# Kernel optimization log

Hardware: AMD Instinct MI355X
Metric: run time of the kernel (lower is better)

The kernel has to match this reference:

```python
import jax, jax.numpy as jnp
import numpy as np

CLASS_EMBED_DIM = 128
TOPK = 64
EPS = float(np.finfo(float).eps)
ALPHA = 0.99


def setup_inputs() -> dict:
    key = jax.random.key(0)
    k1, k2, k3 = jax.random.split(key, 3)
    b, n, d = 16, 256, 640  # d = embed_dim + class_embed_dim
    embed_dim, inner_dim = 512, 512
    x = jax.random.normal(k1, (b, n, d), dtype=jnp.float32)
    # kaiming-normal style init: std = sqrt(2 / fan_in)
    std = (2.0 / embed_dim) ** 0.5
    Wq = jax.random.normal(k2, (embed_dim, inner_dim), dtype=jnp.float32) * std
    Wk = jax.random.normal(k3, (embed_dim, inner_dim), dtype=jnp.float32) * std
    alpha = jnp.float32(ALPHA)
    return {"x": x, "Wq": Wq, "Wk": Wk, "alpha": alpha}


def reference(x, Wq, Wk, alpha):
    b, n, d = x.shape
    xf = x.reshape(b * n, d)            # (N, embed+class)
    xe = xf[:, :-CLASS_EMBED_DIM]       # (N, embed)
    q = xe @ Wq                         # (N, inner)
    k = xe @ Wk                         # (N, inner)
    D = q.shape[1]
    # dots[i,j] = mean_d (q_i - k_j)^2, via expansion (avoids N x N x D tensor)
    q2 = jnp.sum(q * q, axis=1)
    k2 = jnp.sum(k * k, axis=1)
    dots = (q2[:, None] + k2[None, :] - 2.0 * (q @ k.T)) / D  # (N, N)
    N = dots.shape[0]
    _, idx = jax.lax.top_k(dots, TOPK)  # largest, matching torch.topk
    mask = jnp.zeros_like(dots).at[jnp.arange(N)[:, None], idx].set(1.0)
    mask = ((mask + mask.T) > 0).astype(jnp.float32)
    attn = dots * mask
    A = jnp.eye(N, dtype=dots.dtype) - alpha * attn + EPS
    out = jnp.linalg.inv(A) @ xf        # (N, d); to_v is identity
    return out.reshape(b, n, d)
```

## Files before the change

### kernel.cpp

```cpp
#include <hip/hip_runtime.h>
#include <float.h>

#define NN 4096
#define DD 640
#define DE 512
#define NB 16
#define OB 128
#define NOB (NN/OB)
#define SB 128
#define NSB (NN/SB)

static __device__ __forceinline__ float4 ldg4(const float* p) { return *(const float4*)p; }

__global__ __launch_bounds__(256) void proj_gemm(
    const float* __restrict__ xf, const float* __restrict__ Wq,
    const float* __restrict__ Wk, float* __restrict__ q, float* __restrict__ kk_)
{
  __shared__ float Xs[32][68], Qs[32][68], Ks[32][68];
  const int i0 = blockIdx.x * 64, c0 = blockIdx.y * 64;
  const int t = threadIdx.x, tr = t >> 4, tc = t & 15;
  float accq[4][4] = {}, acck[4][4] = {};
  for (int kb = 0; kb < DE; kb += 32) {
    {
      int m = t >> 3, k4 = (t & 7) << 2;
      float4 v0 = ldg4(xf + (size_t)(i0 + m) * DD + kb + k4);
      float4 v1 = ldg4(xf + (size_t)(i0 + m + 32) * DD + kb + k4);
      Xs[k4+0][m] = v0.x; Xs[k4+1][m] = v0.y; Xs[k4+2][m] = v0.z; Xs[k4+3][m] = v0.w;
      Xs[k4+0][m+32] = v1.x; Xs[k4+1][m+32] = v1.y; Xs[k4+2][m+32] = v1.z; Xs[k4+3][m+32] = v1.w;
    }
    {
      int kr = t >> 3, n8 = (t & 7) << 3;
      *(float4*)&Qs[kr][n8]   = ldg4(Wq + (size_t)(kb + kr) * DE + c0 + n8);
      *(float4*)&Qs[kr][n8+4] = ldg4(Wq + (size_t)(kb + kr) * DE + c0 + n8 + 4);
      *(float4*)&Ks[kr][n8]   = ldg4(Wk + (size_t)(kb + kr) * DE + c0 + n8);
      *(float4*)&Ks[kr][n8+4] = ldg4(Wk + (size_t)(kb + kr) * DE + c0 + n8 + 4);
    }
    __syncthreads();
    #pragma unroll
    for (int kkk = 0; kkk < 32; ++kkk) {
      float a[4], bq[4], bk[4];
      *(float4*)a  = *(const float4*)&Xs[kkk][tr << 2];
      *(float4*)bq = *(const float4*)&Qs[kkk][tc << 2];
      *(float4*)bk = *(const float4*)&Ks[kkk][tc << 2];
      #pragma unroll
      for (int r = 0; r < 4; ++r)
        #pragma unroll
        for (int c = 0; c < 4; ++c) { accq[r][c] += a[r]*bq[c]; acck[r][c] += a[r]*bk[c]; }
    }
    __syncthreads();
  }
  #pragma unroll
  for (int r = 0; r < 4; ++r) {
    float* qp = q   + (size_t)(i0 + (tr<<2) + r) * DE + c0 + (tc<<2);
    float* kp = kk_ + (size_t)(i0 + (tr<<2) + r) * DE + c0 + (tc<<2);
    *(float4*)qp = make_float4(accq[r][0], accq[r][1], accq[r][2], accq[r][3]);
    *(float4*)kp = make_float4(acck[r][0], acck[r][1], acck[r][2], acck[r][3]);
  }
}

__global__ __launch_bounds__(256) void rownorm(
    const float* __restrict__ q, const float* __restrict__ kk_,
    float* __restrict__ q2, float* __restrict__ k2)
{
  int w = (blockIdx.x * 256 + threadIdx.x) >> 6;
  int lane = threadIdx.x & 63;
  const float* src = (w < NN) ? q : kk_;
  int row = (w < NN) ? w : w - NN;
  const float* p = src + (size_t)row * DE;
  float s = 0.f;
  for (int c = lane; c < DE; c += 64) { float v = p[c]; s += v * v; }
  for (int off = 32; off; off >>= 1) s += __shfl_down(s, off);
  if (lane == 0) { if (w < NN) q2[row] = s; else k2[row] = s; }
}

__global__ __launch_bounds__(256) void dots_gemm(
    const float* __restrict__ q, const float* __restrict__ kk_,
    const float* __restrict__ q2, const float* __restrict__ k2,
    float* __restrict__ dots)
{
  __shared__ float Qs[32][68], Ks[32][68];
  const int i0 = blockIdx.x * 64, j0 = blockIdx.y * 64;
  const int t = threadIdx.x, tr = t >> 4, tc = t & 15;
  float acc[4][4] = {};
  for (int kb = 0; kb < DE; kb += 32) {
    int m = t >> 3, k4 = (t & 7) << 2;
    {
      float4 v0 = ldg4(q + (size_t)(i0 + m) * DE + kb + k4);
      float4 v1 = ldg4(q + (size_t)(i0 + m + 32) * DE + kb + k4);
      Qs[k4+0][m] = v0.x; Qs[k4+1][m] = v0.y; Qs[k4+2][m] = v0.z; Qs[k4+3][m] = v0.w;
      Qs[k4+0][m+32] = v1.x; Qs[k4+1][m+32] = v1.y; Qs[k4+2][m+32] = v1.z; Qs[k4+3][m+32] = v1.w;
    }
    {
      float4 v0 = ldg4(kk_ + (size_t)(j0 + m) * DE + kb + k4);
      float4 v1 = ldg4(kk_ + (size_t)(j0 + m + 32) * DE + kb + k4);
      Ks[k4+0][m] = v0.x; Ks[k4+1][m] = v0.y; Ks[k4+2][m] = v0.z; Ks[k4+3][m] = v0.w;
      Ks[k4+0][m+32] = v1.x; Ks[k4+1][m+32] = v1.y; Ks[k4+2][m+32] = v1.z; Ks[k4+3][m+32] = v1.w;
    }
    __syncthreads();
    #pragma unroll
    for (int kkk = 0; kkk < 32; ++kkk) {
      float a[4], b[4];
      *(float4*)a = *(const float4*)&Qs[kkk][tr << 2];
      *(float4*)b = *(const float4*)&Ks[kkk][tc << 2];
      #pragma unroll
      for (int r = 0; r < 4; ++r)
        #pragma unroll
        for (int c = 0; c < 4; ++c) acc[r][c] += a[r]*b[c];
    }
    __syncthreads();
  }
  const float inv = 1.0f / (float)DE;
  float k2v[4]; *(float4*)k2v = ldg4(k2 + j0 + (tc<<2));
  #pragma unroll
  for (int r = 0; r < 4; ++r) {
    float q2v = q2[i0 + (tr<<2) + r];
    float o[4];
    #pragma unroll
    for (int c = 0; c < 4; ++c) o[c] = (q2v + k2v[c] - 2.0f*acc[r][c]) * inv;
    *(float4*)(dots + (size_t)(i0 + (tr<<2) + r) * NN + j0 + (tc<<2)) =
        make_float4(o[0], o[1], o[2], o[3]);
  }
}

__global__ __launch_bounds__(256) void topk_bits(
    const float* __restrict__ dots, unsigned int* __restrict__ bits)
{
  __shared__ float row[NN];
  __shared__ unsigned int b[128];
  __shared__ float rv[4]; __shared__ int ri[4];
  const int i = blockIdx.x, t = threadIdx.x;
  const float* dr = dots + (size_t)i * NN;
  for (int c = t; c < NN; c += 256) row[c] = dr[c];
  if (t < 128) b[t] = 0u;
  __syncthreads();
  for (int it = 0; it < 64; ++it) {
    float bv = -FLT_MAX; int bi = NN;
    for (int c = t; c < NN; c += 256) { float v = row[c]; if (v > bv) { bv = v; bi = c; } }
    for (int off = 32; off; off >>= 1) {
      float ov = __shfl_down(bv, off); int oi = __shfl_down(bi, off);
      if (ov > bv || (ov == bv && oi < bi)) { bv = ov; bi = oi; }
    }
    if ((t & 63) == 0) { rv[t >> 6] = bv; ri[t >> 6] = bi; }
    __syncthreads();
    if (t == 0) {
      float fv = rv[0]; int fi = ri[0];
      for (int w = 1; w < 4; ++w)
        if (rv[w] > fv || (rv[w] == fv && ri[w] < fi)) { fv = rv[w]; fi = ri[w]; }
      b[fi >> 5] |= 1u << (fi & 31);
      row[fi] = -FLT_MAX;
    }
    __syncthreads();
  }
  if (t < 128) bits[(size_t)i * 128 + t] = b[t];
}

__global__ __launch_bounds__(256) void build_A(
    float* __restrict__ A, const unsigned int* __restrict__ bits,
    const float* __restrict__ alpha_p)
{
  int tid = blockIdx.x * 256 + threadIdx.x;
  int i = tid >> 10;
  int j4 = (tid & 1023) << 2;
  float alpha = alpha_p[0];
  float* p = A + (size_t)i * NN + j4;
  float4 d = *(float4*)p;
  unsigned int wrow = bits[(size_t)i * 128 + (j4 >> 5)];
  float dv[4] = {d.x, d.y, d.z, d.w}, o[4];
  #pragma unroll
  for (int u = 0; u < 4; ++u) {
    int j = j4 + u;
    unsigned int m1 = (wrow >> (j & 31)) & 1u;
    unsigned int m2 = (bits[(size_t)j * 128 + (i >> 5)] >> (i & 31)) & 1u;
    float base = (i == j) ? 1.0f : 0.0f;
    o[u] = base - ((m1 | m2) ? alpha * dv[u] : 0.0f);
  }
  *(float4*)p = make_float4(o[0], o[1], o[2], o[3]);
}

__global__ __launch_bounds__(1024) void lu_panel(
    float* __restrict__ A, int k0, int ok0, int* __restrict__ piv)
{
  const int t = threadIdx.x;
  const int M = NN - k0;
  float a[4][NB];
  __shared__ float bufA[NB], bufB[NB];
  __shared__ float rv[16]; __shared__ int ri[16];
  __shared__ int s_pr;
  __shared__ int piv_s[NB];
  __shared__ int sd[32], ss[32];
  __shared__ float l16[16][17];
  __shared__ float gbuf[32][112];

  #pragma unroll
  for (int i = 0; i < 4; ++i) {
    int r = t + (i << 10);
    if (r < M) {
      const float* src = A + (size_t)(k0 + r) * NN + k0;
      #pragma unroll
      for (int c4 = 0; c4 < NB; c4 += 4) {
        float4 v = ldg4(src + c4);
        a[i][c4] = v.x; a[i][c4+1] = v.y; a[i][c4+2] = v.z; a[i][c4+3] = v.w;
      }
    }
  }

  #pragma unroll
  for (int j = 0; j < NB; ++j) {
    float bv = -1.0f; int br = 1 << 30;
    #pragma unroll
    for (int i = 0; i < 4; ++i) {
      int r = t + (i << 10);
      if (r >= j && r < M) {
        float v = fabsf(a[i][j]);
        if (v > bv || (v == bv && r < br)) { bv = v; br = r; }
      }
    }
    for (int off = 32; off; off >>= 1) {
      float ov = __shfl_down(bv, off); int orr = __shfl_down(br, off);
      if (ov > bv || (ov == bv && orr < br)) { bv = ov; br = orr; }
    }
    if ((t & 63) == 0) { rv[t >> 6] = bv; ri[t >> 6] = br; }
    __syncthreads();
    if (t == 0) {
      float fv = rv[0]; int fr = ri[0];
      for (int w = 1; w < 16; ++w)
        if (rv[w] > fv || (rv[w] == fv && ri[w] < fr)) { fv = rv[w]; fr = ri[w]; }
      s_pr = fr; piv_s[j] = k0 + fr;
    }
    __syncthreads();
    const int pr = s_pr, prT = pr & 1023, prS = pr >> 10;
    if (t == prT) {
      #pragma unroll
      for (int i2 = 0; i2 < 4; ++i2) if (i2 == prS) {
        #pragma unroll
        for (int c = 0; c < NB; ++c) bufB[c] = a[i2][c];
      }
    }
    if (t == j) {
      #pragma unroll
      for (int c = 0; c < NB; ++c) bufA[c] = a[0][c];
    }
    __syncthreads();
    if (t == j) {
      #pragma unroll
      for (int c = 0; c < NB; ++c) a[0][c] = bufB[c];
    }
    if (t == prT) {
      #pragma unroll
      for (int i2 = 0; i2 < 4; ++i2) if (i2 == prS) {
        #pragma unroll
        for (int c = 0; c < NB; ++c) a[i2][c] = bufA[c];
      }
    }
    float rp = 1.0f / bufB[j];
    #pragma unroll
    for (int i = 0; i < 4; ++i) {
      int r = t + (i << 10);
      if (r > j && r < M) {
        float mlt = a[i][j] * rp;
        a[i][j] = mlt;
        #pragma unroll
        for (int c = j + 1; c < NB; ++c) a[i][c] -= mlt * bufB[c];
      }
    }
    __syncthreads();
  }

  #pragma unroll
  for (int i = 0; i < 4; ++i) {
    int r = t + (i << 10);
    if (r < M) {
      float* dst = A + (size_t)(k0 + r) * NN + k0;
      #pragma unroll
      for (int c4 = 0; c4 < NB; c4 += 4)
        *(float4*)(dst + c4) = make_float4(a[i][c4], a[i][c4+1], a[i][c4+2], a[i][c4+3]);
    }
  }
  if (t < NB) piv[k0 + t] = piv_s[t];

  if (t < 16) {
    #pragma unroll
    for (int c2 = 0; c2 < NB; ++c2) l16[t][c2] = a[0][c2];
  }

  if (t < 32) {
    int slotrow = (t < NB) ? (k0 + t) : -1;
    int content = slotrow;
    int next_ext = NB;
    for (int j = 0; j < NB; ++j) {
      int p = piv_s[j];
      unsigned long long mask = __ballot(slotrow == p);
      int bslot;
      if (mask) bslot = __ffsll((unsigned long long)mask) - 1;
      else {
        bslot = next_ext;
        if (t == next_ext) { slotrow = p; content = p; }
        next_ext++;
      }
      int srcl = (t == j) ? bslot : ((t == bslot) ? j : t);
      content = __shfl(content, srcl);
    }
    sd[t] = slotrow;
    ss[t] = content;
  }
  __syncthreads();

  const int p16 = k0 - ok0;
  for (int idx = t; idx < 32 * 112; idx += 1024) {
    int i = idx / 112, cc = idx - i * 112;
    if (sd[i] >= 0 && sd[i] != ss[i]) {
      int c = ok0 + (cc < p16 ? cc : cc + NB);
      gbuf[i][cc] = A[(size_t)ss[i] * NN + c];
    }
  }
  __syncthreads();
  for (int idx = t; idx < 32 * 112; idx += 1024) {
    int i = idx / 112, cc = idx - i * 112;
    if (sd[i] >= 0 && sd[i] != ss[i]) {
      int c = ok0 + (cc < p16 ? cc : cc + NB);
      A[(size_t)sd[i] * NN + c] = gbuf[i][cc];
    }
  }
  __syncthreads();

  const int w = ok0 + OB - (k0 + NB);
  if (t < w) {
    int c = k0 + NB + t;
    int cc = p16 + t;
    float x[16];
    #pragma unroll
    for (int i = 0; i < 16; ++i)
      x[i] = (ss[i] != sd[i]) ? gbuf[i][cc] : A[(size_t)(k0 + i) * NN + c];
    #pragma unroll
    for (int i = 1; i < 16; ++i)
      #pragma unroll
      for (int j = 0; j < i; ++j) x[i] -= l16[i][j] * x[j];
    #pragma unroll
    for (int i = 0; i < 16; ++i) A[(size_t)(k0 + i) * NN + c] = x[i];
  }
}

__global__ __launch_bounds__(64) void net_perm128(
    const int* __restrict__ piv_g, int ok0,
    int* __restrict__ nd, int* __restrict__ ns)
{
  __shared__ int pl[OB];
  const int L = threadIdx.x;
  pl[L] = piv_g[ok0 + L];
  pl[L + 64] = piv_g[ok0 + 64 + L];
  __syncthreads();
  int c0 = ok0 + L, c1 = ok0 + 64 + L, c2 = -1, c3 = -1;
  int sr2 = -1, sr3 = -1;
  int next_ext = 128;
  for (int j = 0; j < OB; ++j) {
    int p = pl[j];
    int s2;
    if (p < ok0 + OB) s2 = p - ok0;
    else {
      unsigned long long m2 = __ballot(sr2 == p);
      unsigned long long m3 = __ballot(sr3 == p);
      if (m2) s2 = 128 + (__ffsll(m2) - 1);
      else if (m3) s2 = 192 + (__ffsll(m3) - 1);
      else {
        s2 = next_ext;
        if (s2 < 192) { if (L == s2 - 128) { sr2 = p; c2 = p; } }
        else          { if (L == s2 - 192) { sr3 = p; c3 = p; } }
        next_ext++;
      }
    }
    int jp = j >> 6, jl = j & 63, sp = s2 >> 6, sl = s2 & 63;
    int vj0 = __shfl(c0, jl), vj1 = __shfl(c1, jl);
    int vj = (jp == 0) ? vj0 : vj1;
    int vs0 = __shfl(c0, sl), vs1 = __shfl(c1, sl), vs2 = __shfl(c2, sl), vs3 = __shfl(c3, sl);
    int vs = (sp == 0) ? vs0 : (sp == 1) ? vs1 : (sp == 2) ? vs2 : vs3;
    if (jp == 0 && L == jl) c0 = vs;
    if (jp == 1 && L == jl) c1 = vs;
    if (sp == 0 && L == sl) c0 = vj;
    if (sp == 1 && L == sl) c1 = vj;
    if (sp == 2 && L == sl) c2 = vj;
    if (sp == 3 && L == sl) c3 = vj;
  }
  nd[L] = ok0 + L;        ns[L] = c0;
  nd[64 + L] = ok0 + 64 + L; ns[64 + L] = c1;
  nd[128 + L] = sr2;      ns[128 + L] = c2;
  nd[192 + L] = sr3;      ns[192 + L] = c3;
}

__global__ __launch_bounds__(256) void perm_copy_out(
    const float* __restrict__ A, float* __restrict__ T,
    const int* __restrict__ nd, const int* __restrict__ ns, int ok0)
{
  int s = blockIdx.y;
  int d = nd[s], sr = ns[s];
  if (d < 0 || d == sr) return;
  int c = blockIdx.x * 1024 + threadIdx.x * 4;
  if (c >= ok0 && c < ok0 + OB) return;
  *(float4*)(T + (size_t)s * NN + c) = ldg4(A + (size_t)sr * NN + c);
}

__global__ __launch_bounds__(256) void perm_copy_in(
    float* __restrict__ A, const float* __restrict__ T,
    const int* __restrict__ nd, const int* __restrict__ ns, int ok0)
{
  int s = blockIdx.y;
  int d = nd[s], sr = ns[s];
  if (d < 0 || d == sr) return;
  int c = blockIdx.x * 1024 + threadIdx.x * 4;
  if (c >= ok0 && c < ok0 + OB) return;
  *(float4*)(A + (size_t)d * NN + c) = ldg4(T + (size_t)s * NN + c);
}

__global__ __launch_bounds__(64) void trsm128L(float* __restrict__ A, int ok0)
{
  __shared__ float Ls[64][65];
  __shared__ float xs[64][133];
  const int t = threadIdx.x;
  const int c = ok0 + OB + blockIdx.x * 64 + t;
  for (int i = 0; i < 128; ++i) xs[t][i] = A[(size_t)(ok0 + i) * NN + c];
  for (int i = 0; i < 64; ++i) Ls[i][t] = A[(size_t)(ok0 + i) * NN + ok0 + t];
  __syncthreads();
  for (int i = 1; i < 64; ++i) {
    float s0 = 0.f, s1 = 0.f, s2 = 0.f, s3 = 0.f;
    int j = 0;
    for (; j + 3 < i; j += 4) {
      s0 += Ls[i][j+0] * xs[t][j+0]; s1 += Ls[i][j+1] * xs[t][j+1];
      s2 += Ls[i][j+2] * xs[t][j+2]; s3 += Ls[i][j+3] * xs[t][j+3];
    }
    for (; j < i; ++j) s0 += Ls[i][j] * xs[t][j];
    xs[t][i] -= (s0 + s1) + (s2 + s3);
  }
  __syncthreads();
  for (int i = 0; i < 64; ++i) Ls[i][t] = A[(size_t)(ok0 + 64 + i) * NN + ok0 + t];
  __syncthreads();
  for (int i = 0; i < 64; ++i) {
    float s0 = 0.f, s1 = 0.f, s2 = 0.f, s3 = 0.f;
    #pragma unroll 4
    for (int j = 0; j < 64; j += 4) {
      s0 += Ls[i][j+0] * xs[t][j+0]; s1 += Ls[i][j+1] * xs[t][j+1];
      s2 += Ls[i][j+2] * xs[t][j+2]; s3 += Ls[i][j+3] * xs[t][j+3];
    }
    xs[t][64 + i] -= (s0 + s1) + (s2 + s3);
  }
  __syncthreads();
  for (int i = 0; i < 64; ++i) Ls[i][t] = A[(size_t)(ok0 + 64 + i) * NN + ok0 + 64 + t];
  __syncthreads();
  for (int i = 1; i < 64; ++i) {
    float s0 = 0.f, s1 = 0.f, s2 = 0.f, s3 = 0.f;
    int j = 0;
    for (; j + 3 < i; j += 4) {
      s0 += Ls[i][j+0] * xs[t][64+j+0]; s1 += Ls[i][j+1] * xs[t][64+j+1];
      s2 += Ls[i][j+2] * xs[t][64+j+2]; s3 += Ls[i][j+3] * xs[t][64+j+3];
    }
    for (; j < i; ++j) s0 += Ls[i][j] * xs[t][64+j];
    xs[t][64 + i] -= (s0 + s1) + (s2 + s3);
  }
  for (int i = 0; i < 128; ++i) A[(size_t)(ok0 + i) * NN + c] = xs[t][i];
}

__global__ __launch_bounds__(256) void rank_update(
    float* __restrict__ C, int ldc,
    const float* __restrict__ Aop, int lda,
    const float* __restrict__ Bop, int ldb,
    int Mr, int Nc, int K)
{
  __shared__ float As[16][68], Bs[16][68];
  const int m0 = blockIdx.x * 64, n0 = blockIdx.y * 64;
  const int t = threadIdx.x, tr = t >> 4, tc = t & 15;
  const float4 z4 = make_float4(0.f, 0.f, 0.f, 0.f);
  float acc[4][4] = {};
  for (int kb = 0; kb < K; kb += 16) {
    {
      int m = t >> 2, k4 = (t & 3) << 2;
      float4 v0 = (m0 + m < Mr) ? ldg4(Aop + (size_t)(m0 + m) * lda + kb + k4) : z4;
      As[k4+0][m] = v0.x; As[k4+1][m] = v0.y; As[k4+2][m] = v0.z; As[k4+3][m] = v0.w;
    }
    {
      int kr = t >> 4, n4 = (t & 15) << 2;
      bool ok = (n0 + n4 < Nc);
      float4 w0 = ok ? ldg4(Bop + (size_t)(kb + kr) * ldb + n0 + n4) : z4;
      *(float4*)&Bs[kr][n4] = w0;
    }
    __syncthreads();
    #pragma unroll
    for (int kkk = 0; kkk < 16; ++kkk) {
      float a[4], b[4];
      *(float4*)a = *(const float4*)&As[kkk][tr << 2];
      *(float4*)b = *(const float4*)&Bs[kkk][tc << 2];
      #pragma unroll
      for (int r = 0; r < 4; ++r)
        #pragma unroll
        for (int c = 0; c < 4; ++c) acc[r][c] += a[r] * b[c];
    }
    __syncthreads();
  }
  #pragma unroll
  for (int r = 0; r < 4; ++r) {
    int m = m0 + (tr << 2) + r;
    int n = n0 + (tc << 2);
    if (m < Mr && n < Nc) {
      float* cp = C + (size_t)m * ldc + n;
      float4 cv = *(float4*)cp;
      cv.x -= acc[r][0]; cv.y -= acc[r][1]; cv.z -= acc[r][2]; cv.w -= acc[r][3];
      *(float4*)cp = cv;
    }
  }
}

__global__ __launch_bounds__(256) void rank_update128(
    float* __restrict__ C, int ldc,
    const float* __restrict__ Aop, int lda,
    const float* __restrict__ Bop, int ldb,
    int K)
{
  __shared__ float As[16][132], Bs[16][132];
  const int m0 = blockIdx.x * 128, n0 = blockIdx.y * 128;
  const int t = threadIdx.x;
  const int tr = t >> 4, tc = t & 15;
  float acc[8][8] = {};
  for (int kb = 0; kb < K; kb += 16) {
    {
      int m = t >> 1, k8 = (t & 1) << 3;
      const float* ap = Aop + (size_t)(m0 + m) * lda + kb + k8;
      float4 v0 = ldg4(ap), v1 = ldg4(ap + 4);
      As[k8+0][m] = v0.x; As[k8+1][m] = v0.y; As[k8+2][m] = v0.z; As[k8+3][m] = v0.w;
      As[k8+4][m] = v1.x; As[k8+5][m] = v1.y; As[k8+6][m] = v1.z; As[k8+7][m] = v1.w;
    }
    {
      int kr = t >> 4, c8 = (t & 15) << 3;
      const float* bp = Bop + (size_t)(kb + kr) * ldb + n0 + c8;
      *(float4*)&Bs[kr][c8]     = ldg4(bp);
      *(float4*)&Bs[kr][c8 + 4] = ldg4(bp + 4);
    }
    __syncthreads();
    #pragma unroll
    for (int k = 0; k < 16; ++k) {
      float av[8], bv[8];
      *(float4*)av       = *(const float4*)&As[k][tr << 3];
      *(float4*)(av + 4) = *(const float4*)&As[k][(tr << 3) + 4];
      *(float4*)bv       = *(const float4*)&Bs[k][tc << 3];
      *(float4*)(bv + 4) = *(const float4*)&Bs[k][(tc << 3) + 4];
      #pragma unroll
      for (int r = 0; r < 8; ++r)
        #pragma unroll
        for (int c = 0; c < 8; ++c) acc[r][c] += av[r] * bv[c];
    }
    __syncthreads();
  }
  #pragma unroll
  for (int r = 0; r < 8; ++r) {
    float* cp = C + (size_t)(m0 + (tr << 3) + r) * ldc + n0 + (tc << 3);
    float4 c0 = *(float4*)cp, c1 = *(float4*)(cp + 4);
    c0.x -= acc[r][0]; c0.y -= acc[r][1]; c0.z -= acc[r][2]; c0.w -= acc[r][3];
    c1.x -= acc[r][4]; c1.y -= acc[r][5]; c1.z -= acc[r][6]; c1.w -= acc[r][7];
    *(float4*)cp = c0; *(float4*)(cp + 4) = c1;
  }
}

__global__ __launch_bounds__(128) void inv_tri(
    const float* __restrict__ Ag, float* __restrict__ invT, int upper)
{
  __shared__ float xs[128][128];
  const int s = blockIdx.x, t = threadIdx.x;
  const size_t r0 = (size_t)s * SB;
  for (int i = 0; i < 128; ++i) xs[i][t] = 0.0f;
  const float* Tb = Ag + r0 * NN + r0;
  if (!upper) {
    xs[t][t] = 1.0f;
    for (int i = 1; i < 128; ++i) {
      float s0 = 0.f, s1 = 0.f, s2 = 0.f, s3 = 0.f;
      int j = 0;
      for (; j + 3 < i; j += 4) {
        s0 += Tb[(size_t)i * NN + j+0] * xs[j+0][t];
        s1 += Tb[(size_t)i * NN + j+1] * xs[j+1][t];
        s2 += Tb[(size_t)i * NN + j+2] * xs[j+2][t];
        s3 += Tb[(size_t)i * NN + j+3] * xs[j+3][t];
      }
      for (; j < i; ++j) s0 += Tb[(size_t)i * NN + j] * xs[j][t];
      float ssum = (s0 + s1) + (s2 + s3);
      if (i != t) xs[i][t] = -ssum;
    }
  } else {
    xs[t][t] = 1.0f / Tb[(size_t)t * NN + t];
    for (int i = 126; i >= 0; --i) {
      float s0 = 0.f, s1 = 0.f, s2 = 0.f, s3 = 0.f;
      int j = i + 1;
      for (; j + 3 < 128; j += 4) {
        s0 += Tb[(size_t)i * NN + j+0] * xs[j+0][t];
        s1 += Tb[(size_t)i * NN + j+1] * xs[j+1][t];
        s2 += Tb[(size_t)i * NN + j+2] * xs[j+2][t];
        s3 += Tb[(size_t)i * NN + j+3] * xs[j+3][t];
      }
      for (; j < 128; ++j) s0 += Tb[(size_t)i * NN + j] * xs[j][t];
      float ssum = (s0 + s1) + (s2 + s3);
      if (i != t) xs[i][t] = -ssum / Tb[(size_t)i * NN + i];
    }
  }
  for (int i = 0; i < 128; ++i) invT[(size_t)s * SB * SB + (size_t)i * SB + t] = xs[i][t];
}

__global__ __launch_bounds__(1024) void perm_compose(
    const int* __restrict__ piv, int* __restrict__ idxp)
{
  __shared__ int pl[NN];
  const int t = threadIdx.x;
  for (int j = t; j < NN; j += 1024) pl[j] = piv[j];
  __syncthreads();
  int pos[4] = { t, t + 1024, t + 2048, t + 3072 };
  for (int j = NN - 1; j >= 0; --j) {
    int p = pl[j];
    #pragma unroll
    for (int u = 0; u < 4; ++u) {
      int r = t + (u << 10);
      if (j <= r) {
        if (pos[u] == j) pos[u] = p;
        else if (pos[u] == p) pos[u] = j;
      }
    }
  }
  #pragma unroll
  for (int u = 0; u < 4; ++u) idxp[t + (u << 10)] = pos[u];
}

__global__ __launch_bounds__(256) void gather_rows(
    const float* __restrict__ xf, const int* __restrict__ idxp, float* __restrict__ out)
{
  const int r = blockIdx.x, t = threadIdx.x;
  const int src = idxp[r];
  const float4* s = (const float4*)(xf + (size_t)src * DD);
  float4* d = (float4*)(out + (size_t)r * DD);
  for (int c = t; c < DD / 4; c += 256) d[c] = s[c];
}

__global__ __launch_bounds__(256) void diag_apply(
    float* __restrict__ B, const float* __restrict__ Minv, int r0)
{
  __shared__ float Bs[128][68];
  const int c0 = blockIdx.x * 64, t = threadIdx.x;
  #pragma unroll
  for (int v = 0; v < 8; ++v) {
    int id = t + v * 256;
    int k = id >> 4, c4 = (id & 15) << 2;
    *(float4*)&Bs[k][c4] = ldg4(B + (size_t)(r0 + k) * DD + c0 + c4);
  }
  __syncthreads();
  const int tr = t >> 4, tc = t & 15;
  float acc[8][4] = {};
  for (int k4 = 0; k4 < 128; k4 += 4) {
    float b0[4], b1[4], b2[4], b3[4];
    *(float4*)b0 = *(const float4*)&Bs[k4+0][tc << 2];
    *(float4*)b1 = *(const float4*)&Bs[k4+1][tc << 2];
    *(float4*)b2 = *(const float4*)&Bs[k4+2][tc << 2];
    *(float4*)b3 = *(const float4*)&Bs[k4+3][tc << 2];
    #pragma unroll
    for (int rr = 0; rr < 8; ++rr) {
      float m[4]; *(float4*)m = ldg4(Minv + (size_t)(tr*8 + rr) * SB + k4);
      #pragma unroll
      for (int c = 0; c < 4; ++c)
        acc[rr][c] += m[0]*b0[c] + m[1]*b1[c] + m[2]*b2[c] + m[3]*b3[c];
    }
  }
  #pragma unroll
  for (int rr = 0; rr < 8; ++rr)
    *(float4*)(B + (size_t)(r0 + tr*8 + rr) * DD + c0 + (tc << 2)) =
        make_float4(acc[rr][0], acc[rr][1], acc[rr][2], acc[rr][3]);
}

extern "C" void kernel_launch(void* const* d_in, const int* in_sizes, int n_in,
                              void* d_out, int out_size, void* d_ws, size_t ws_size,
                              hipStream_t stream)
{
  const float* xf    = (const float*)d_in[0];
  const float* Wq    = (const float*)d_in[1];
  const float* Wk    = (const float*)d_in[2];
  const float* alpha = (const float*)d_in[3];
  float* out = (float*)d_out;
  char* ws = (char*)d_ws;

  float* Amat = (float*)(ws);
  float* q    = (float*)(ws + 67108864ull);
  float* kbuf = (float*)(ws + 75497472ull);
  float* invL = (float*)(ws + 83886080ull);
  float* invU = (float*)(ws + 85983232ull);
  unsigned int* bits = (unsigned int*)(ws + 88080384ull);
  float* q2   = (float*)(ws + 90177536ull);
  float* k2   = (float*)(ws + 90193920ull);
  int* piv    = (int*)(ws + 90210304ull);
  int* idxp   = (int*)(ws + 90226688ull);
  int* nd     = (int*)(ws + 90243072ull);
  int* ns     = (int*)(ws + 90275840ull);
  float* Tbuf = q;

  proj_gemm<<<dim3(NN/64, DE/64), 256, 0, stream>>>(xf, Wq, Wk, q, kbuf);
  rownorm<<<2 * NN / 4, 256, 0, stream>>>(q, kbuf, q2, k2);
  dots_gemm<<<dim3(NN/64, NN/64), 256, 0, stream>>>(q, kbuf, q2, k2, Amat);
  topk_bits<<<NN, 256, 0, stream>>>(Amat, bits);
  build_A<<<NN * NN / 4 / 256, 256, 0, stream>>>(Amat, bits, alpha);

  for (int ob = 0; ob < NOB; ++ob) {
    const int ok0 = ob * OB;
    for (int p = 0; p < OB / NB; ++p) {
      const int k0 = ok0 + p * NB;
      lu_panel<<<1, 1024, 0, stream>>>(Amat, k0, ok0, piv);
      if (p < OB / NB - 1) {
        const int k1 = k0 + NB;
        const int w = ok0 + OB - k1;
        const int M2 = NN - k1;
        rank_update<<<dim3((M2 + 63) / 64, (w + 63) / 64), 256, 0, stream>>>(
            Amat + (size_t)k1 * NN + k1, NN,
            Amat + (size_t)k1 * NN + k0, NN,
            Amat + (size_t)k0 * NN + k1, NN,
            M2, w, NB);
      }
    }
    net_perm128<<<1, 64, 0, stream>>>(piv, ok0, nd, ns);
    perm_copy_out<<<dim3(NN / 1024, 256), 256, 0, stream>>>(Amat, Tbuf, nd, ns, ok0);
    perm_copy_in<<<dim3(NN / 1024, 256), 256, 0, stream>>>(Amat, Tbuf, nd, ns, ok0);
    const int b1 = ok0 + OB;
    const int M2 = NN - b1;
    if (M2 > 0) {
      trsm128L<<<M2 / 64, 64, 0, stream>>>(Amat, ok0);
      rank_update128<<<dim3(M2 / 128, M2 / 128), 256, 0, stream>>>(
          Amat + (size_t)b1 * NN + b1, NN,
          Amat + (size_t)b1 * NN + ok0, NN,
          Amat + (size_t)ok0 * NN + b1, NN,
          OB);
    }
  }

  inv_tri<<<NSB, 128, 0, stream>>>(Amat, invL, 0);
  inv_tri<<<NSB, 128, 0, stream>>>(Amat, invU, 1);
  perm_compose<<<1, 1024, 0, stream>>>(piv, idxp);
  gather_rows<<<NN, 256, 0, stream>>>(xf, idxp, out);

  for (int s = 0; s < NSB; ++s) {
    int r0 = s * SB;
    diag_apply<<<DD / 64, 256, 0, stream>>>(out, invL + (size_t)s * SB * SB, r0);
    if (r0 + SB < NN) {
      int M2 = NN - r0 - SB;
      rank_update128<<<dim3(M2 / 128, DD / 128), 256, 0, stream>>>(
          out + (size_t)(r0 + SB) * DD, DD,
          Amat + (size_t)(r0 + SB) * NN + r0, NN,
          out + (size_t)r0 * DD, DD,
          SB);
    }
  }
  for (int s = NSB - 1; s >= 0; --s) {
    int r0 = s * SB;
    diag_apply<<<DD / 64, 256, 0, stream>>>(out, invU + (size_t)s * SB * SB, r0);
    if (r0 > 0) {
      rank_update128<<<dim3(r0 / 128, DD / 128), 256, 0, stream>>>(
          out, DD,
          Amat + r0, NN,
          out + (size_t)r0 * DD, DD,
          SB);
    }
  }
}
```

Measured before the change: 41.26 ms.

## Fold inner-panel rank updates into lu_panel as left-looking updates

Drops the separate rank_update launch between 16-wide sub-panels inside each 128 outer block. Instead, lu_panel applies the prior sub-panels' updates to its own columns left-looking, and also to the U row block before its triangular solve. It also removes one barrier per pivot step by double-buffering the reduction and pivot-row buffers and having every thread do the final argmax. This cuts kernel launch count and synchronisation, but makes the single-block panel kernel do more serial work as the sub-panel index grows.

```diff
diff --git a/kernel.cpp b/kernel.cpp
--- a/kernel.cpp
+++ b/kernel.cpp
@@ -182,13 +182,16 @@
 {
   const int t = threadIdx.x;
   const int M = NN - k0;
+  const int p16 = k0 - ok0;
+  const int nq = p16 / NB;
   float a[4][NB];
-  __shared__ float bufA[NB], bufB[NB];
-  __shared__ float rv[16]; __shared__ int ri[16];
-  __shared__ int s_pr;
+  __shared__ float rv[2][16]; __shared__ int ri[2][16];
+  __shared__ float pb[2][NB];
+  __shared__ float bufA[2][NB];
   __shared__ int piv_s[NB];
   __shared__ int sd[32], ss[32];
   __shared__ float l16[16][17];
+  __shared__ float us[16][17];
   __shared__ float gbuf[32][112];
 
   #pragma unroll
@@ -204,8 +207,36 @@
     }
   }
 
+  for (int q = 0; q < nq; ++q) {
+    const int kq = ok0 + q * NB;
+    if (t < 256) us[t >> 4][t & 15] = A[(size_t)(kq + (t >> 4)) * NN + k0 + (t & 15)];
+    __syncthreads();
+    #pragma unroll
+    for (int i = 0; i < 4; ++i) {
+      int r = t + (i << 10);
+      if (r < M) {
+        const float* lp = A + (size_t)(k0 + r) * NN + kq;
+        float l[16];
+        #pragma unroll
+        for (int c4 = 0; c4 < NB; c4 += 4) {
+          float4 v = ldg4(lp + c4);
+          l[c4] = v.x; l[c4+1] = v.y; l[c4+2] = v.z; l[c4+3] = v.w;
+        }
+        #pragma unroll
+        for (int c = 0; c < NB; ++c) {
+          float s = 0.f;
+          #pragma unroll
+          for (int k = 0; k < NB; ++k) s += l[k] * us[k][c];
+          a[i][c] -= s;
+        }
+      }
+    }
+    __syncthreads();
+  }
+
   #pragma unroll
   for (int j = 0; j < NB; ++j) {
+    const int bb = j & 1;
     float bv = -1.0f; int br = 1 << 30;
     #pragma unroll
     for (int i = 0; i < 4; ++i) {
@@ -219,40 +250,39 @@
       float ov = __shfl_down(bv, off); int orr = __shfl_down(br, off);
       if (ov > bv || (ov == bv && orr < br)) { bv = ov; br = orr; }
     }
-    if ((t & 63) == 0) { rv[t >> 6] = bv; ri[t >> 6] = br; }
-    __syncthreads();
-    if (t == 0) {
-      float fv = rv[0]; int fr = ri[0];
-      for (int w = 1; w < 16; ++w)
-        if (rv[w] > fv || (rv[w] == fv && ri[w] < fr)) { fv = rv[w]; fr = ri[w]; }
-      s_pr = fr; piv_s[j] = k0 + fr;
-    }
-    __syncthreads();
-    const int pr = s_pr, prT = pr & 1023, prS = pr >> 10;
+    if ((t & 63) == 0) { rv[bb][t >> 6] = bv; ri[bb][t >> 6] = br; }
+    __syncthreads();
+    float fv = rv[bb][0]; int fr = ri[bb][0];
+    #pragma unroll
+    for (int w = 1; w < 16; ++w)
+      if (rv[bb][w] > fv || (rv[bb][w] == fv && ri[bb][w] < fr)) { fv = rv[bb][w]; fr = ri[bb][w]; }
+    const int pr = fr;
+    if (t == 0) piv_s[j] = k0 + pr;
+    const int prT = pr & 1023, prS = pr >> 10;
     if (t == prT) {
       #pragma unroll
       for (int i2 = 0; i2 < 4; ++i2) if (i2 == prS) {
         #pragma unroll
-        for (int c = 0; c < NB; ++c) bufB[c] = a[i2][c];
+        for (int c = 0; c < NB; ++c) pb[bb][c] = a[i2][c];
       }
     }
     if (t == j) {
       #pragma unroll
-      for (int c = 0; c < NB; ++c) bufA[c] = a[0][c];
+      for (int c = 0; c < NB; ++c) bufA[bb][c] = a[0][c];
     }
     __syncthreads();
     if (t == j) {
       #pragma unroll
-      for (int c = 0; c < NB; ++c) a[0][c] = bufB[c];
+      for (int c = 0; c < NB; ++c) a[0][c] = pb[bb][c];
     }
     if (t == prT) {
       #pragma unroll
       for (int i2 = 0; i2 < 4; ++i2) if (i2 == prS) {
         #pragma unroll
-        for (int c = 0; c < NB; ++c) a[i2][c] = bufA[c];
-      }
-    }
-    float rp = 1.0f / bufB[j];
+        for (int c = 0; c < NB; ++c) a[i2][c] = bufA[bb][c];
+      }
+    }
+    float rp = 1.0f / pb[bb][j];
     #pragma unroll
     for (int i = 0; i < 4; ++i) {
       int r = t + (i << 10);
@@ -260,11 +290,11 @@
         float mlt = a[i][j] * rp;
         a[i][j] = mlt;
         #pragma unroll
-        for (int c = j + 1; c < NB; ++c) a[i][c] -= mlt * bufB[c];
-      }
-    }
-    __syncthreads();
-  }
+        for (int c = j + 1; c < NB; ++c) a[i][c] -= mlt * pb[bb][c];
+      }
+    }
+  }
+  __syncthreads();
 
   #pragma unroll
   for (int i = 0; i < 4; ++i) {
@@ -305,7 +335,6 @@
   }
   __syncthreads();
 
-  const int p16 = k0 - ok0;
   for (int idx = t; idx < 32 * 112; idx += 1024) {
     int i = idx / 112, cc = idx - i * 112;
     if (sd[i] >= 0 && sd[i] != ss[i]) {
@@ -324,19 +353,46 @@
   __syncthreads();
 
   const int w = ok0 + OB - (k0 + NB);
-  if (t < w) {
-    int c = k0 + NB + t;
-    int cc = p16 + t;
+  if (w > 0) {
+    const int c = k0 + NB + t;
+    const int cc = p16 + t;
+    const bool own = (t < w);
     float x[16];
-    #pragma unroll
-    for (int i = 0; i < 16; ++i)
-      x[i] = (ss[i] != sd[i]) ? gbuf[i][cc] : A[(size_t)(k0 + i) * NN + c];
-    #pragma unroll
-    for (int i = 1; i < 16; ++i)
-      #pragma unroll
-      for (int j = 0; j < i; ++j) x[i] -= l16[i][j] * x[j];
-    #pragma unroll
-    for (int i = 0; i < 16; ++i) A[(size_t)(k0 + i) * NN + c] = x[i];
+    if (own) {
+      #pragma unroll
+      for (int i = 0; i < 16; ++i)
+        x[i] = (ss[i] != sd[i]) ? gbuf[i][cc] : A[(size_t)(k0 + i) * NN + c];
+    }
+    for (int q = 0; q < nq; ++q) {
+      const int kq = ok0 + q * NB;
+      if (t < 256) {
+        int i = t >> 4, k = t & 15;
+        us[i][k] = (ss[i] != sd[i]) ? gbuf[i][16 * q + k]
+                                    : A[(size_t)(k0 + i) * NN + kq + k];
+      }
+      __syncthreads();
+      if (own) {
+        float uv[16];
+        #pragma unroll
+        for (int k = 0; k < 16; ++k) uv[k] = A[(size_t)(kq + k) * NN + c];
+        #pragma unroll
+        for (int i = 0; i < 16; ++i) {
+          float s = 0.f;
+          #pragma unroll
+          for (int k = 0; k < 16; ++k) s += us[i][k] * uv[k];
+          x[i] -= s;
+        }
+      }
+      __syncthreads();
+    }
+    if (own) {
+      #pragma unroll
+      for (int i = 1; i < 16; ++i)
+        #pragma unroll
+        for (int j = 0; j < i; ++j) x[i] -= l16[i][j] * x[j];
+      #pragma unroll
+      for (int i = 0; i < 16; ++i) A[(size_t)(k0 + i) * NN + c] = x[i];
+    }
   }
 }
 
@@ -457,55 +513,6 @@
   for (int i = 0; i < 128; ++i) A[(size_t)(ok0 + i) * NN + c] = xs[t][i];
 }
 
-__global__ __launch_bounds__(256) void rank_update(
-    float* __restrict__ C, int ldc,
-    const float* __restrict__ Aop, int lda,
-    const float* __restrict__ Bop, int ldb,
-    int Mr, int Nc, int K)
-{
-  __shared__ float As[16][68], Bs[16][68];
-  const int m0 = blockIdx.x * 64, n0 = blockIdx.y * 64;
-  const int t = threadIdx.x, tr = t >> 4, tc = t & 15;
-  const float4 z4 = make_float4(0.f, 0.f, 0.f, 0.f);
-  float acc[4][4] = {};
-  for (int kb = 0; kb < K; kb += 16) {
-    {
-      int m = t >> 2, k4 = (t & 3) << 2;
-      float4 v0 = (m0 + m < Mr) ? ldg4(Aop + (size_t)(m0 + m) * lda + kb + k4) : z4;
-      As[k4+0][m] = v0.x; As[k4+1][m] = v0.y; As[k4+2][m] = v0.z; As[k4+3][m] = v0.w;
-    }
-    {
-      int kr = t >> 4, n4 = (t & 15) << 2;
-      bool ok = (n0 + n4 < Nc);
-      float4 w0 = ok ? ldg4(Bop + (size_t)(kb + kr) * ldb + n0 + n4) : z4;
-      *(float4*)&Bs[kr][n4] = w0;
-    }
-    __syncthreads();
-    #pragma unroll
-    for (int kkk = 0; kkk < 16; ++kkk) {
-      float a[4], b[4];
-      *(float4*)a = *(const float4*)&As[kkk][tr << 2];
-      *(float4*)b = *(const float4*)&Bs[kkk][tc << 2];
-      #pragma unroll
-      for (int r = 0; r < 4; ++r)
-        #pragma unroll
-        for (int c = 0; c < 4; ++c) acc[r][c] += a[r] * b[c];
-    }
-    __syncthreads();
-  }
-  #pragma unroll
-  for (int r = 0; r < 4; ++r) {
-    int m = m0 + (tr << 2) + r;
-    int n = n0 + (tc << 2);
-    if (m < Mr && n < Nc) {
-      float* cp = C + (size_t)m * ldc + n;
-      float4 cv = *(float4*)cp;
-      cv.x -= acc[r][0]; cv.y -= acc[r][1]; cv.z -= acc[r][2]; cv.w -= acc[r][3];
-      *(float4*)cp = cv;
-    }
-  }
-}
-
 __global__ __launch_bounds__(256) void rank_update128(
     float* __restrict__ C, int ldc,
     const float* __restrict__ Aop, int lda,
@@ -701,16 +708,6 @@
     for (int p = 0; p < OB / NB; ++p) {
       const int k0 = ok0 + p * NB;
       lu_panel<<<1, 1024, 0, stream>>>(Amat, k0, ok0, piv);
-      if (p < OB / NB - 1) {
-        const int k1 = k0 + NB;
-        const int w = ok0 + OB - k1;
-        const int M2 = NN - k1;
-        rank_update<<<dim3((M2 + 63) / 64, (w + 63) / 64), 256, 0, stream>>>(
-            Amat + (size_t)k1 * NN + k1, NN,
-            Amat + (size_t)k1 * NN + k0, NN,
-            Amat + (size_t)k0 * NN + k1, NN,
-            M2, w, NB);
-      }
     }
     net_perm128<<<1, 64, 0, stream>>>(piv, ok0, nd, ns);
     perm_copy_out<<<dim3(NN / 1024, 256), 256, 0, stream>>>(Amat, Tbuf, nd, ns, ok0);
```

Result: slower. 52.09 ms (+26.3%).
